# Kernel optimization log

Measured on AMD Instinct MI355X. Metric: run time of the kernel, lower is better.

## Reference

```python
import jax, jax.numpy as jnp
import numpy as np
from jax import lax

N_RAYS, N_STEPS, G = 4096, 160, 160
COLOR_DIM, WIDTH = 3, 128
POS_PE, VIEW_PE = 5, 4
XYZ_MIN, XYZ_MAX = -1.0, 1.0
NEAR = 0.05
STEPSIZE = 0.5
VOXEL_SIZE = (XYZ_MAX - XYZ_MIN) / G
DIST = STEPSIZE * VOXEL_SIZE
S_VAL = 80.0
FASTCOLOR_THRES = 1e-7
MASK_THRES = 1e-3
ALPHA_INIT = 1e-4
ACT_SHIFT = float(np.log(1.0 / (1.0 - ALPHA_INIT) - 1.0))
SMOOTH_K, SMOOTH_SIGMA = 5, 1.0
POSFREQ = jnp.asarray([2.0 ** i for i in range(POS_PE)], jnp.float32)
VIEWFREQ = jnp.asarray([2.0 ** i for i in range(VIEW_PE)], jnp.float32)


def _gauss_kernel():
    ax = np.arange(SMOOTH_K) - SMOOTH_K // 2
    g = np.exp(-(ax ** 2) / (2.0 * SMOOTH_SIGMA ** 2))
    k = g[:, None, None] * g[None, :, None] * g[None, None, :]
    return jnp.asarray(k / k.sum(), np.float32)[None, None]


def _trilerp(grid, pts):
    # grid [C,Gx,Gx,Gx]; pts [...,3] in world coords -> [..., C] (align_corners trilinear)
    Gx = grid.shape[-1]
    u = (pts - XYZ_MIN) / (XYZ_MAX - XYZ_MIN) * (Gx - 1)
    u = jnp.clip(u, 0.0, Gx - 1.0)
    i0 = jnp.clip(jnp.floor(u).astype(jnp.int32), 0, Gx - 2)
    f = u - i0.astype(u.dtype)
    x0, y0, z0 = i0[..., 0], i0[..., 1], i0[..., 2]
    fx, fy, fz = f[..., 0], f[..., 1], f[..., 2]
    def g8(ix, iy, iz):
        return grid[:, ix, iy, iz]  # [C, ...]
    out = (g8(x0, y0, z0) * (1 - fx) * (1 - fy) * (1 - fz)
         + g8(x0, y0, z0 + 1) * (1 - fx) * (1 - fy) * fz
         + g8(x0, y0 + 1, z0) * (1 - fx) * fy * (1 - fz)
         + g8(x0, y0 + 1, z0 + 1) * (1 - fx) * fy * fz
         + g8(x0 + 1, y0, z0) * fx * (1 - fy) * (1 - fz)
         + g8(x0 + 1, y0, z0 + 1) * fx * (1 - fy) * fz
         + g8(x0 + 1, y0 + 1, z0) * fx * fy * (1 - fz)
         + g8(x0 + 1, y0 + 1, z0 + 1) * fx * fy * fz)
    return jnp.moveaxis(out, 0, -1)


def _alphas2weights(alpha):
    # per-ray (segmented) exclusive cumprod of transmittance; alpha [N,S]
    T = jnp.cumprod(1.0 - alpha, axis=1)
    T_excl = jnp.concatenate([jnp.ones_like(T[:, :1]), T[:, :-1]], axis=1)
    return alpha * T_excl, T[:, -1]


def _mlp(x, w0, b0, w1, b1, w2, b2):
    h = jax.nn.relu(x @ w0 + b0)
    h = jax.nn.relu(h @ w1 + b1)
    return h @ w2 + b2


def _forward(rays_o, rays_d, viewdirs, sdf_grid, mask_density,
             off_color_grid, emo_color_grid,
             off_w0, off_b0, off_w1, off_b1, off_w2, off_b2,
             emo_w0, emo_b0, emo_w1, emo_b1, emo_w2, emo_b2, em_modes):
    N = rays_o.shape[0]
    t = NEAR + DIST * jnp.arange(N_STEPS, dtype=jnp.float32)
    ray_pts = rays_o[:, None, :] + rays_d[:, None, :] * t[None, :, None]  # [N,S,3]

    # MaskCache: threshold alpha from coarse density grid (boolean keep mask)
    dens = _trilerp(mask_density, ray_pts)[..., 0]
    mask_alpha = 1.0 - jnp.exp(-jax.nn.softplus(dens + ACT_SHIFT) * DIST)
    keep0 = mask_alpha >= MASK_THRES  # [N,S]

    # Gaussian-smoothed SDF grid + central-difference gradient grid
    sdf_s = lax.conv_general_dilated(sdf_grid, _gauss_kernel(), (1, 1, 1), 'SAME',
                                     dimension_numbers=('NCDHW', 'OIDHW', 'NCDHW'))[0]  # [1,G,G,G]
    s = sdf_s[0]
    grad_grid = jnp.zeros((3, G, G, G), sdf_grid.dtype)
    grad_grid = grad_grid.at[0, 1:-1].set((s[2:] - s[:-2]) / (2 * VOXEL_SIZE))
    grad_grid = grad_grid.at[1, :, 1:-1].set((s[:, 2:] - s[:, :-2]) / (2 * VOXEL_SIZE))
    grad_grid = grad_grid.at[2, :, :, 1:-1].set((s[:, :, 2:] - s[:, :, :-2]) / (2 * VOXEL_SIZE))

    sdf = _trilerp(sdf_s, ray_pts)[..., 0]   # [N,S]
    gradient = _trilerp(grad_grid, ray_pts)  # [N,S,3]

    # NeuS alpha from sdf (scatter, grad variant, cos_anneal = 1)
    true_cos = jnp.einsum('nd,nsd->ns', viewdirs, gradient)
    iter_cos = -jax.nn.relu(-true_cos)
    prev_cdf = jax.nn.sigmoid((sdf - iter_cos * DIST * 0.5) * S_VAL)
    next_cdf = jax.nn.sigmoid((sdf + iter_cos * DIST * 0.5) * S_VAL)
    alpha = jnp.clip((prev_cdf - next_cdf + 1e-5) / (prev_cdf + 1e-5), 0.0, 1.0)
    alpha = jnp.where(keep0, alpha, 0.0)  # masked points contribute nothing

    weights, _ = _alphas2weights(alpha)
    keep1 = weights > FASTCOLOR_THRES
    alpha = jnp.where(keep1, alpha, 0.0)
    weights, alphainv_last = _alphas2weights(alpha)

    # features: pos PE, view PE (per-ray, gathered by ray_id == broadcast), normal
    rays_xyz = (ray_pts - XYZ_MIN) / (XYZ_MAX - XYZ_MIN)  # [N,S,3]
    xyz_emb = (rays_xyz[..., None] * POSFREQ).reshape(N, N_STEPS, -1)
    v_emb = (viewdirs[..., None] * VIEWFREQ).reshape(N, -1)
    v_full = jnp.concatenate([v_emb, jnp.sin(v_emb), jnp.cos(v_emb)], -1)
    v_full = jnp.broadcast_to(v_full[:, None, :], (N, N_STEPS, v_full.shape[-1]))
    normal = gradient / (jnp.linalg.norm(gradient, axis=-1, keepdims=True) + 1e-5)
    rgb_feat = jnp.concatenate([rays_xyz, jnp.sin(xyz_emb), jnp.cos(xyz_emb), v_full, normal], -1)

    off_in = jnp.concatenate([_trilerp(off_color_grid, ray_pts), rgb_feat], -1)
    emo_in = jnp.concatenate([_trilerp(emo_color_grid, ray_pts), rgb_feat], -1)
    off_rgb = jax.nn.sigmoid(_mlp(off_in, off_w0, off_b0, off_w1, off_b1, off_w2, off_b2))
    emo_rgb = jax.nn.sigmoid(_mlp(emo_in, emo_w0, emo_b0, emo_w1, emo_b1, emo_w2, emo_b2))
    on_mask = (em_modes == 1)[:, None, None]  # em_modes[ray_id] == 1
    rgb = jnp.where(on_mask, emo_rgb, 0.0) + off_rgb

    w_ = weights[..., None]
    rgb_marched = jnp.sum(w_ * rgb, axis=1)  # segment_coo(sum over ray_id)
    cum_weights = jnp.sum(w_, axis=1)        # [N,1]
    return rgb_marched, alphainv_last, 1.0 - cum_weights


def setup_inputs() -> dict:
    key = jax.random.key(0)
    ks = jax.random.split(key, 12)
    rays_o = jax.random.uniform(ks[0], (N_RAYS, 3), jnp.float32, -0.3, 0.3)
    rd = jax.random.normal(ks[1], (N_RAYS, 3), jnp.float32)
    rays_d = rd / jnp.linalg.norm(rd, axis=-1, keepdims=True)
    viewdirs = rays_d
    em_modes = jax.random.randint(ks[2], (N_RAYS,), 0, 2)
    lin = np.linspace(-1.0, 1.0, G, dtype=np.float32)
    x, y, z = np.meshgrid(lin, lin, lin, indexing='ij')
    sdf_grid = jnp.asarray(np.sqrt(x ** 2 + y ** 2 + z ** 2) - 1.0)[None, None]  # sphere-SDF init
    mask_density = jax.random.normal(ks[3], (1, 80, 80, 80), jnp.float32) * 2.0 + 12.0
    off_color_grid = jax.random.normal(ks[4], (COLOR_DIM, G, G, G), jnp.float32) * 0.1
    emo_color_grid = jax.random.normal(ks[5], (COLOR_DIM, G, G, G), jnp.float32) * 0.1
    DIM0 = 3 + 3 * POS_PE * 2 + 3 * VIEW_PE * 3 + COLOR_DIM + 3  # = 75
    def lw(k, i, o):
        return jax.random.normal(k, (i, o), jnp.float32) * (1.0 / np.sqrt(i))
    return dict(rays_o=rays_o, rays_d=rays_d, viewdirs=viewdirs, em_modes=em_modes,
                sdf_grid=sdf_grid, mask_density=mask_density,
                off_color_grid=off_color_grid, emo_color_grid=emo_color_grid,
                off_w0=lw(ks[6], DIM0, WIDTH), off_b0=jnp.zeros((WIDTH,), jnp.float32),
                off_w1=lw(ks[7], WIDTH, WIDTH), off_b1=jnp.zeros((WIDTH,), jnp.float32),
                off_w2=lw(ks[8], WIDTH, 3), off_b2=jnp.zeros((3,), jnp.float32),
                emo_w0=lw(ks[9], DIM0, WIDTH), emo_b0=jnp.zeros((WIDTH,), jnp.float32),
                emo_w1=lw(ks[10], WIDTH, WIDTH), emo_b1=jnp.zeros((WIDTH,), jnp.float32),
                emo_w2=lw(ks[11], WIDTH, 3), emo_b2=jnp.zeros((3,), jnp.float32))


def reference(rays_o, rays_d, viewdirs, em_modes, sdf_grid, mask_density,
              off_color_grid, emo_color_grid,
              off_w0, off_b0, off_w1, off_b1, off_w2, off_b2,
              emo_w0, emo_b0, emo_w1, emo_b1, emo_w2, emo_b2):
    return _forward(rays_o, rays_d, viewdirs, sdf_grid, mask_density,
                    off_color_grid, emo_color_grid,
                    off_w0, off_b0, off_w1, off_b1, off_w2, off_b2,
                    emo_w0, emo_b0, emo_w1, emo_b1, emo_w2, emo_b2, em_modes)
```

## Files before the change

### kernel.cpp

```cpp
#include <hip/hip_runtime.h>

#define NRAYS 4096
#define NSTEPS 160
#define NSAMP (NRAYS*NSTEPS)
#define GG 160
#define GG2 (GG*GG)
#define GG3 (GG*GG2)
#define GM 80
#define GM2 (GM*GM)

#define NEARV 0.05f
#define DISTV 0.00625f
#define SVAL 80.0f
#define ACT_SHIFT_C (-9.2102403669758813f)
#define INV2H 40.0f
#define MASK_THRES_C 1e-3f
#define FAST_THRES_C 1e-7f

#define KW0 0.05448868454964295f
#define KW1 0.24420134200323332f
#define KW2 0.40261994689424750f

__device__ __forceinline__ float sigmf(float x){ return 1.0f/(1.0f+__expf(-x)); }
__device__ __forceinline__ float softplusf_(float x){ return (x>20.0f)? x : log1pf(__expf(x)); }

__device__ __forceinline__ void tricoord(float p, int Gx, int& i0, float& fr){
  float u = (p + 1.0f)*0.5f*(float)(Gx-1);
  u = fminf(fmaxf(u, 0.0f), (float)(Gx-1));
  int i = (int)floorf(u);
  i = min(max(i,0), Gx-2);
  i0 = i; fr = u - (float)i;
}

__global__ __launch_bounds__(256) void ksmooth_yz(const float* __restrict__ in, float* __restrict__ out,
                                                  float* __restrict__ outbuf, int* __restrict__ cnt){
  __shared__ float S[36][37];
  __shared__ float Tz[36][33];
  const int bx = blockIdx.x;
  const int t = threadIdx.x;
  if (bx == 0){
    for (int i = t; i < NRAYS*3; i += 256) outbuf[i] = 0.0f;
    if (t == 0) *cnt = 0;
  }
  const int x  = bx / 25;
  const int tile = bx % 25;
  const int Y0 = (tile/5)*32, Z0 = (tile%5)*32;
  const float kw[5] = {KW0,KW1,KW2,KW1,KW0};
  for (int i = t; i < 36*36; i += 256){
    int r = i/36, c = i - (i/36)*36;
    int y = Y0 + r - 2, z = Z0 + c - 2;
    float v = 0.0f;
    if (y>=0 && y<GG && z>=0 && z<GG) v = in[(x*GG+y)*GG+z];
    S[r][c] = v;
  }
  __syncthreads();
  for (int i = t; i < 36*32; i += 256){
    int r = i >> 5, c = i & 31;
    float acc = 0.f;
    #pragma unroll
    for (int d=0; d<5; d++) acc += kw[d]*S[r][c+d];
    Tz[r][c] = acc;
  }
  __syncthreads();
  for (int i = t; i < 32*32; i += 256){
    int yy = i >> 5, c = i & 31;
    float acc = 0.f;
    #pragma unroll
    for (int d=0; d<5; d++) acc += kw[d]*Tz[yy+d][c];
    out[(x*GG + Y0+yy)*GG + Z0 + c] = acc;
  }
}

__global__ __launch_bounds__(64) void kmarch(
  const float* __restrict__ ro, const float* __restrict__ rd,
  const float* __restrict__ vd, const float* __restrict__ maskg,
  const float* __restrict__ Y,
  int* __restrict__ slist, float* __restrict__ sw, float* __restrict__ sgrad,
  int* __restrict__ cnt, float* __restrict__ out)
{
  int n = blockIdx.x*64 + threadIdx.x;
  if (n >= NRAYS) return;
  const float ox=ro[n*3+0], oy=ro[n*3+1], oz=ro[n*3+2];
  const float dx=rd[n*3+0], dy=rd[n*3+1], dz=rd[n*3+2];
  const float vx=vd[n*3+0], vy=vd[n*3+1], vz=vd[n*3+2];
  const float kwc[5] = {KW0,KW1,KW2,KW1,KW0};
  float T1=1.0f, T2=1.0f, cum=0.0f;
  for (int s=0; s<NSTEPS; s++){
    float tt = NEARV + DISTV*(float)s;
    float px = ox + dx*tt, py = oy + dy*tt, pz = oz + dz*tt;

    int mx,my,mz; float mfx,mfy,mfz;
    tricoord(px, GM, mx, mfx); tricoord(py, GM, my, mfy); tricoord(pz, GM, mz, mfz);
    int mid = (mx*GM + my)*GM + mz;
    float d000=maskg[mid],        d001=maskg[mid+1];
    float d010=maskg[mid+GM],     d011=maskg[mid+GM+1];
    float d100=maskg[mid+GM2],    d101=maskg[mid+GM2+1];
    float d110=maskg[mid+GM2+GM], d111=maskg[mid+GM2+GM+1];
    float m00 = d000 + (d001-d000)*mfz;
    float m01 = d010 + (d011-d010)*mfz;
    float m10 = d100 + (d101-d100)*mfz;
    float m11 = d110 + (d111-d110)*mfz;
    float m0 = m00 + (m01-m00)*mfy;
    float m1 = m10 + (m11-m10)*mfy;
    float dens = m0 + (m1-m0)*mfx;
    float malpha = 1.0f - __expf(-softplusf_(dens + ACT_SHIFT_C)*DISTV);

    int ix,iy,iz; float fx,fy,fz;
    tricoord(px, GG, ix, fx); tricoord(py, GG, iy, fy); tricoord(pz, GG, iz, fz);

    float R[2][2][8];
    #pragma unroll
    for (int jb=0;jb<2;jb++)
      #pragma unroll
      for (int jc=0;jc<2;jc++)
        #pragma unroll
        for (int j=0;j<8;j++){
          int a = ix-3+j;
          R[jb][jc][j] = (a>=0 && a<GG) ? Y[(a*GG + iy+jb)*GG + iz+jc] : 0.0f;
        }
    const bool hasym = (iy>=1), hasyp = (iy<=GG-3);
    const bool haszm = (iz>=1), haszp = (iz<=GG-3);
    float Eym[2][6], Eyp[2][6], Ezm[2][6], Ezp[2][6];
    #pragma unroll
    for (int jc=0;jc<2;jc++)
      #pragma unroll
      for (int j=0;j<6;j++){
        int a = ix-2+j;
        bool ax = (a>=0 && a<GG);
        Eym[jc][j] = (hasym && ax) ? Y[(a*GG + iy-1)*GG + iz+jc] : 0.0f;
        Eyp[jc][j] = (hasyp && ax) ? Y[(a*GG + iy+2)*GG + iz+jc] : 0.0f;
      }
    #pragma unroll
    for (int jb=0;jb<2;jb++)
      #pragma unroll
      for (int j=0;j<6;j++){
        int a = ix-2+j;
        bool ax = (a>=0 && a<GG);
        Ezm[jb][j] = (haszm && ax) ? Y[(a*GG + iy+jb)*GG + iz-1] : 0.0f;
        Ezp[jb][j] = (haszp && ax) ? Y[(a*GG + iy+jb)*GG + iz+2] : 0.0f;
      }

    float sdf=0.0f, gx=0.0f, gy=0.0f, gz=0.0f;
    #pragma unroll
    for (int ja=0;ja<2;ja++){
      #pragma unroll
      for (int jb=0;jb<2;jb++){
        #pragma unroll
        for (int jc=0;jc<2;jc++){
          float w = (ja?fx:1.0f-fx)*(jb?fy:1.0f-fy)*(jc?fz:1.0f-fz);
          const float* r = R[jb][jc];
          float s0=0.0f;
          #pragma unroll
          for (int t2=0;t2<5;t2++) s0 += kwc[t2]*r[ja+1+t2];
          sdf += w*s0;
          int a = ix+ja, b = iy+jb, c = iz+jc;
          if (a>=1 && a<=GG-2){
            float sp=0.0f, sm=0.0f;
            #pragma unroll
            for (int t2=0;t2<5;t2++){ sp += kwc[t2]*r[ja+2+t2]; sm += kwc[t2]*r[ja+t2]; }
            gx += w*INV2H*(sp-sm);
          }
          if (b>=1 && b<=GG-2){
            float acc=0.0f;
            if (jb==0){
              const float* up = R[1][jc];
              const float* dn = Eym[jc];
              #pragma unroll
              for (int t2=0;t2<5;t2++) acc += kwc[t2]*(up[ja+1+t2] - dn[ja+t2]);
            } else {
              const float* up = Eyp[jc];
              const float* dn = R[0][jc];
              #pragma unroll
              for (int t2=0;t2<5;t2++) acc += kwc[t2]*(up[ja+t2] - dn[ja+1+t2]);
            }
            gy += w*INV2H*acc;
          }
          if (c>=1 && c<=GG-2){
            float acc=0.0f;
            if (jc==0){
              const float* up = R[jb][1];
              const float* dn = Ezm[jb];
              #pragma unroll
              for (int t2=0;t2<5;t2++) acc += kwc[t2]*(up[ja+1+t2] - dn[ja+t2]);
            } else {
              const float* up = Ezp[jb];
              const float* dn = R[jb][0];
              #pragma unroll
              for (int t2=0;t2<5;t2++) acc += kwc[t2]*(up[ja+t2] - dn[ja+1+t2]);
            }
            gz += w*INV2H*acc;
          }
        }
      }
    }

    float tc = vx*gx + vy*gy + vz*gz;
    float icos = fminf(tc, 0.0f);
    float e = icos*DISTV*0.5f;
    float prev = sigmf((sdf - e)*SVAL);
    float nxt  = sigmf((sdf + e)*SVAL);
    float alpha = (prev - nxt + 1e-5f)/(prev + 1e-5f);
    alpha = fminf(fmaxf(alpha, 0.0f), 1.0f);
    if (!(malpha >= MASK_THRES_C)) alpha = 0.0f;

    float w1 = alpha*T1; T1 *= (1.0f - alpha);
    float a2 = (w1 > FAST_THRES_C) ? alpha : 0.0f;
    float wv = a2*T2;   T2 *= (1.0f - a2);
    cum += wv;
    if (wv > 0.0f){
      int pos = atomicAdd(cnt, 1);
      slist[pos] = n*NSTEPS + s;
      sw[pos] = wv;
      sgrad[pos*3+0]=gx; sgrad[pos*3+1]=gy; sgrad[pos*3+2]=gz;
    }
    if (T1 <= FAST_THRES_C) break;
  }
  out[NRAYS*3 + n] = T2;
  out[NRAYS*4 + n] = 1.0f - cum;
}

__global__ __launch_bounds__(256) void kmlp5(
  const float* __restrict__ ro, const float* __restrict__ rd,
  const float* __restrict__ vd, const int* __restrict__ em,
  const float* __restrict__ offc, const float* __restrict__ emoc,
  const int* __restrict__ slist, const float* __restrict__ sw,
  const float* __restrict__ sgrad, const int* __restrict__ cnt,
  const float* __restrict__ W0o, const float* __restrict__ b0o,
  const float* __restrict__ W1o, const float* __restrict__ b1o,
  const float* __restrict__ W2o, const float* __restrict__ b2o,
  const float* __restrict__ W0e, const float* __restrict__ b0e,
  const float* __restrict__ W1e, const float* __restrict__ b1e,
  const float* __restrict__ W2e, const float* __restrict__ b2e,
  float* __restrict__ out)
{
  __shared__ float X[32][80];
  __shared__ float H[32][132];
  __shared__ float H2[32][132];
  __shared__ float OUTB[32][3];
  __shared__ float WSH[32];
  __shared__ float GS[32][3];
  __shared__ int SSAMP[32];
  __shared__ int SEM[32];
  __shared__ int s_go;

  const int t = threadIdx.x;
  const int count = *cnt;
  const int head = blockIdx.x & 1;
  const int cstride = gridDim.x >> 1;

  const float* W0 = head ? W0e : W0o;  const float* b0 = head ? b0e : b0o;
  const float* W1 = head ? W1e : W1o;  const float* b1 = head ? b1e : b1o;
  const float* W2 = head ? W2e : W2o;  const float* b2 = head ? b2e : b2o;
  const float* cg = head ? emoc : offc;
  const float4* W04 = (const float4*)W0;
  const float4* W14 = (const float4*)W1;

  const int lane = t & 31;
  const int sg   = t >> 5;

  for (int chunk = blockIdx.x >> 1; chunk*32 < count; chunk += cstride) {
    const int base = chunk*32;
    if (t == 0) s_go = 0;
    if (t < 32) {
      int i = base + t;
      bool vld = (i < count);
      int samp = vld ? slist[i] : 0;
      SSAMP[t] = samp;
      WSH[t]   = vld ? sw[i] : 0.0f;
      GS[t][0] = vld ? sgrad[i*3+0] : 0.0f;
      GS[t][1] = vld ? sgrad[i*3+1] : 0.0f;
      GS[t][2] = vld ? sgrad[i*3+2] : 0.0f;
      SEM[t]   = vld ? em[samp/NSTEPS] : 0;
    }
    __syncthreads();
    if (t < 32) {
      bool live = (WSH[t] > 0.0f) && (head == 0 || SEM[t] != 0);
      if (live) s_go = 1;
    }
    __syncthreads();

    if (s_go) {
      {
        const int s = t & 31;
        const int r = t >> 5;
        const int samp = SSAMP[s];
        const int n = samp / NSTEPS;
        const int step = samp - n*NSTEPS;
        const float tt = NEARV + DISTV*(float)step;
        const float px = ro[n*3+0] + rd[n*3+0]*tt;
        const float py = ro[n*3+1] + rd[n*3+1]*tt;
        const float pz = ro[n*3+2] + rd[n*3+2]*tt;
        if (r < 3) {
          int ix,iy,iz; float fx,fy,fz;
          tricoord(px, GG, ix, fx); tricoord(py, GG, iy, fy); tricoord(pz, GG, iz, fz);
          const float* g = cg + (size_t)r * GG3;
          const int id = (ix*GG + iy)*GG + iz;
          float v000=g[id],        v001=g[id+1];
          float v010=g[id+GG],     v011=g[id+GG+1];
          float v100=g[id+GG2],    v101=g[id+GG2+1];
          float v110=g[id+GG2+GG], v111=g[id+GG2+GG+1];
          float c00 = v000 + (v001-v000)*fz;
          float c01 = v010 + (v011-v010)*fz;
          float c10 = v100 + (v101-v100)*fz;
          float c11 = v110 + (v111-v110)*fz;
          float c0 = c00 + (c01-c00)*fy;
          float c1 = c10 + (c11-c10)*fy;
          X[s][r] = c0 + (c1-c0)*fx;
        } else if (r == 3) {
          X[s][3] = (px+1.0f)*0.5f;
          X[s][4] = (py+1.0f)*0.5f;
          X[s][5] = (pz+1.0f)*0.5f;
          float gx = GS[s][0], gy = GS[s][1], gz = GS[s][2];
          float inv = 1.0f/(sqrtf(gx*gx+gy*gy+gz*gz)+1e-5f);
          X[s][72] = gx*inv; X[s][73] = gy*inv; X[s][74] = gz*inv;
          X[s][75] = 0.0f; X[s][76] = 0.0f; X[s][77] = 0.0f; X[s][78] = 0.0f; X[s][79] = 0.0f;
        } else if (r < 7) {
          const int a = r - 4;
          const float coord = (a==0)?px:((a==1)?py:pz);
          const float rxyz = (coord+1.0f)*0.5f;
          float fr = 1.0f;
          #pragma unroll
          for (int q = 0; q < 5; q++) {
            float e = rxyz*fr; fr *= 2.0f;
            X[s][6  + a*5 + q] = __sinf(e);
            X[s][21 + a*5 + q] = __cosf(e);
          }
          const float v = vd[n*3+a];
          float fr2 = 1.0f;
          #pragma unroll
          for (int q = 0; q < 4; q++) {
            float e = v*fr2; fr2 *= 2.0f;
            X[s][36 + a*4 + q] = e;
            X[s][48 + a*4 + q] = __sinf(e);
            X[s][60 + a*4 + q] = __cosf(e);
          }
        }
      }
      __syncthreads();

      {
        const float4 bb = ((const float4*)b0)[lane];
        float4 a0 = bb, a1 = bb, a2 = bb, a3 = bb;
        const int s0 = sg*4;
        #pragma unroll 2
        for (int k4 = 0; k4 < 72; k4 += 4){
          float4 w0 = W04[(k4+0)*32 + lane];
          float4 w1 = W04[(k4+1)*32 + lane];
          float4 w2 = W04[(k4+2)*32 + lane];
          float4 w3 = W04[(k4+3)*32 + lane];
          float4 x0 = *(const float4*)&X[s0+0][k4];
          float4 x1 = *(const float4*)&X[s0+1][k4];
          float4 x2 = *(const float4*)&X[s0+2][k4];
          float4 x3 = *(const float4*)&X[s0+3][k4];
          a0.x+=x0.x*w0.x; a0.y+=x0.x*w0.y; a0.z+=x0.x*w0.z; a0.w+=x0.x*w0.w;
          a1.x+=x1.x*w0.x; a1.y+=x1.x*w0.y; a1.z+=x1.x*w0.z; a1.w+=x1.x*w0.w;
          a2.x+=x2.x*w0.x; a2.y+=x2.x*w0.y; a2.z+=x2.x*w0.z; a2.w+=x2.x*w0.w;
          a3.x+=x3.x*w0.x; a3.y+=x3.x*w0.y; a3.z+=x3.x*w0.z; a3.w+=x3.x*w0.w;
          a0.x+=x0.y*w1.x; a0.y+=x0.y*w1.y; a0.z+=x0.y*w1.z; a0.w+=x0.y*w1.w;
          a1.x+=x1.y*w1.x; a1.y+=x1.y*w1.y; a1.z+=x1.y*w1.z; a1.w+=x1.y*w1.w;
          a2.x+=x2.y*w1.x; a2.y+=x2.y*w1.y; a2.z+=x2.y*w1.z; a2.w+=x2.y*w1.w;
          a3.x+=x3.y*w1.x; a3.y+=x3.y*w1.y; a3.z+=x3.y*w1.z; a3.w+=x3.y*w1.w;
          a0.x+=x0.z*w2.x; a0.y+=x0.z*w2.y; a0.z+=x0.z*w2.z; a0.w+=x0.z*w2.w;
          a1.x+=x1.z*w2.x; a1.y+=x1.z*w2.y; a1.z+=x1.z*w2.z; a1.w+=x1.z*w2.w;
          a2.x+=x2.z*w2.x; a2.y+=x2.z*w2.y; a2.z+=x2.z*w2.z; a2.w+=x2.z*w2.w;
          a3.x+=x3.z*w2.x; a3.y+=x3.z*w2.y; a3.z+=x3.z*w2.z; a3.w+=x3.z*w2.w;
          a0.x+=x0.w*w3.x; a0.y+=x0.w*w3.y; a0.z+=x0.w*w3.z; a0.w+=x0.w*w3.w;
          a1.x+=x1.w*w3.x; a1.y+=x1.w*w3.y; a1.z+=x1.w*w3.z; a1.w+=x1.w*w3.w;
          a2.x+=x2.w*w3.x; a2.y+=x2.w*w3.y; a2.z+=x2.w*w3.z; a2.w+=x2.w*w3.w;
          a3.x+=x3.w*w3.x; a3.y+=x3.w*w3.y; a3.z+=x3.w*w3.z; a3.w+=x3.w*w3.w;
        }
        #pragma unroll
        for (int k = 72; k < 75; k++){
          float4 w = W04[k*32 + lane];
          float x0 = X[s0+0][k], x1 = X[s0+1][k], x2 = X[s0+2][k], x3 = X[s0+3][k];
          a0.x+=x0*w.x; a0.y+=x0*w.y; a0.z+=x0*w.z; a0.w+=x0*w.w;
          a1.x+=x1*w.x; a1.y+=x1*w.y; a1.z+=x1*w.z; a1.w+=x1*w.w;
          a2.x+=x2*w.x; a2.y+=x2*w.y; a2.z+=x2*w.z; a2.w+=x2*w.w;
          a3.x+=x3*w.x; a3.y+=x3*w.y; a3.z+=x3*w.z; a3.w+=x3*w.w;
        }
        H[s0+0][lane*4+0]=fmaxf(a0.x,0.f); H[s0+0][lane*4+1]=fmaxf(a0.y,0.f);
        H[s0+0][lane*4+2]=fmaxf(a0.z,0.f); H[s0+0][lane*4+3]=fmaxf(a0.w,0.f);
        H[s0+1][lane*4+0]=fmaxf(a1.x,0.f); H[s0+1][lane*4+1]=fmaxf(a1.y,0.f);
        H[s0+1][lane*4+2]=fmaxf(a1.z,0.f); H[s0+1][lane*4+3]=fmaxf(a1.w,0.f);
        H[s0+2][lane*4+0]=fmaxf(a2.x,0.f); H[s0+2][lane*4+1]=fmaxf(a2.y,0.f);
        H[s0+2][lane*4+2]=fmaxf(a2.z,0.f); H[s0+2][lane*4+3]=fmaxf(a2.w,0.f);
        H[s0+3][lane*4+0]=fmaxf(a3.x,0.f); H[s0+3][lane*4+1]=fmaxf(a3.y,0.f);
        H[s0+3][lane*4+2]=fmaxf(a3.z,0.f); H[s0+3][lane*4+3]=fmaxf(a3.w,0.f);
      }
      __syncthreads();

      {
        const float4 bb = ((const float4*)b1)[lane];
        float4 a0 = bb, a1 = bb, a2 = bb, a3 = bb;
        const int s0 = sg*4;
        #pragma unroll 2
        for (int k4 = 0; k4 < 128; k4 += 4){
          float4 w0 = W14[(k4+0)*32 + lane];
          float4 w1 = W14[(k4+1)*32 + lane];
          float4 w2 = W14[(k4+2)*32 + lane];
          float4 w3 = W14[(k4+3)*32 + lane];
          float4 x0 = *(const float4*)&H[s0+0][k4];
          float4 x1 = *(const float4*)&H[s0+1][k4];
          float4 x2 = *(const float4*)&H[s0+2][k4];
          float4 x3 = *(const float4*)&H[s0+3][k4];
          a0.x+=x0.x*w0.x; a0.y+=x0.x*w0.y; a0.z+=x0.x*w0.z; a0.w+=x0.x*w0.w;
          a1.x+=x1.x*w0.x; a1.y+=x1.x*w0.y; a1.z+=x1.x*w0.z; a1.w+=x1.x*w0.w;
          a2.x+=x2.x*w0.x; a2.y+=x2.x*w0.y; a2.z+=x2.x*w0.z; a2.w+=x2.x*w0.w;
          a3.x+=x3.x*w0.x; a3.y+=x3.x*w0.y; a3.z+=x3.x*w0.z; a3.w+=x3.x*w0.w;
          a0.x+=x0.y*w1.x; a0.y+=x0.y*w1.y; a0.z+=x0.y*w1.z; a0.w+=x0.y*w1.w;
          a1.x+=x1.y*w1.x; a1.y+=x1.y*w1.y; a1.z+=x1.y*w1.z; a1.w+=x1.y*w1.w;
          a2.x+=x2.y*w1.x; a2.y+=x2.y*w1.y; a2.z+=x2.y*w1.z; a2.w+=x2.y*w1.w;
          a3.x+=x3.y*w1.x; a3.y+=x3.y*w1.y; a3.z+=x3.y*w1.z; a3.w+=x3.y*w1.w;
          a0.x+=x0.z*w2.x; a0.y+=x0.z*w2.y; a0.z+=x0.z*w2.z; a0.w+=x0.z*w2.w;
          a1.x+=x1.z*w2.x; a1.y+=x1.z*w2.y; a1.z+=x1.z*w2.z; a1.w+=x1.z*w2.w;
          a2.x+=x2.z*w2.x; a2.y+=x2.z*w2.y; a2.z+=x2.z*w2.z; a2.w+=x2.z*w2.w;
          a3.x+=x3.z*w2.x; a3.y+=x3.z*w2.y; a3.z+=x3.z*w2.z; a3.w+=x3.z*w2.w;
          a0.x+=x0.w*w3.x; a0.y+=x0.w*w3.y; a0.z+=x0.w*w3.z; a0.w+=x0.w*w3.w;
          a1.x+=x1.w*w3.x; a1.y+=x1.w*w3.y; a1.z+=x1.w*w3.z; a1.w+=x1.w*w3.w;
          a2.x+=x2.w*w3.x; a2.y+=x2.w*w3.y; a2.z+=x2.w*w3.z; a2.w+=x2.w*w3.w;
          a3.x+=x3.w*w3.x; a3.y+=x3.w*w3.y; a3.z+=x3.w*w3.z; a3.w+=x3.w*w3.w;
        }
        H2[s0+0][lane*4+0]=fmaxf(a0.x,0.f); H2[s0+0][lane*4+1]=fmaxf(a0.y,0.f);
        H2[s0+0][lane*4+2]=fmaxf(a0.z,0.f); H2[s0+0][lane*4+3]=fmaxf(a0.w,0.f);
        H2[s0+1][lane*4+0]=fmaxf(a1.x,0.f); H2[s0+1][lane*4+1]=fmaxf(a1.y,0.f);
        H2[s0+1][lane*4+2]=fmaxf(a1.z,0.f); H2[s0+1][lane*4+3]=fmaxf(a1.w,0.f);
        H2[s0+2][lane*4+0]=fmaxf(a2.x,0.f); H2[s0+2][lane*4+1]=fmaxf(a2.y,0.f);
        H2[s0+2][lane*4+2]=fmaxf(a2.z,0.f); H2[s0+2][lane*4+3]=fmaxf(a2.w,0.f);
        H2[s0+3][lane*4+0]=fmaxf(a3.x,0.f); H2[s0+3][lane*4+1]=fmaxf(a3.y,0.f);
        H2[s0+3][lane*4+2]=fmaxf(a3.z,0.f); H2[s0+3][lane*4+3]=fmaxf(a3.w,0.f);
      }
      __syncthreads();

      {
        const int s0 = sg*4;
        #pragma unroll
        for (int i = 0; i < 4; i++){
          const int s = s0 + i;
          float4 h = *(const float4*)&H2[s][lane*4];
          float c0 = h.x*W2[(lane*4+0)*3+0] + h.y*W2[(lane*4+1)*3+0]
                   + h.z*W2[(lane*4+2)*3+0] + h.w*W2[(lane*4+3)*3+0];
          float c1 = h.x*W2[(lane*4+0)*3+1] + h.y*W2[(lane*4+1)*3+1]
                   + h.z*W2[(lane*4+2)*3+1] + h.w*W2[(lane*4+3)*3+1];
          float c2 = h.x*W2[(lane*4+0)*3+2] + h.y*W2[(lane*4+1)*3+2]
                   + h.z*W2[(lane*4+2)*3+2] + h.w*W2[(lane*4+3)*3+2];
          #pragma unroll
          for (int d=16; d>=1; d>>=1){
            c0 += __shfl_down(c0, d, 32);
            c1 += __shfl_down(c1, d, 32);
            c2 += __shfl_down(c2, d, 32);
          }
          if (lane == 0){
            OUTB[s][0] = sigmf(c0 + b2[0]);
            OUTB[s][1] = sigmf(c1 + b2[1]);
            OUTB[s][2] = sigmf(c2 + b2[2]);
          }
        }
      }
      __syncthreads();

      if (t < 96) {
        int s2 = t/3, c = t - s2*3;
        float w = WSH[s2];
        if (w > 0.0f && (head == 0 || SEM[s2] != 0)) {
          int n2 = SSAMP[s2]/NSTEPS;
          atomicAdd(&out[n2*3 + c], w * OUTB[s2][c]);
        }
      }
    }
    __syncthreads();
  }
}

extern "C" void kernel_launch(void* const* d_in, const int* in_sizes, int n_in,
                              void* d_out, int out_size, void* d_ws, size_t ws_size,
                              hipStream_t stream) {
  const float* ro    = (const float*)d_in[0];
  const float* rd    = (const float*)d_in[1];
  const float* vd    = (const float*)d_in[2];
  const int*   em    = (const int*)d_in[3];
  const float* sdfg  = (const float*)d_in[4];
  const float* maskg = (const float*)d_in[5];
  const float* offc  = (const float*)d_in[6];
  const float* emoc  = (const float*)d_in[7];
  const float* W0o = (const float*)d_in[8];
  const float* b0o = (const float*)d_in[9];
  const float* W1o = (const float*)d_in[10];
  const float* b1o = (const float*)d_in[11];
  const float* W2o = (const float*)d_in[12];
  const float* b2o = (const float*)d_in[13];
  const float* W0e = (const float*)d_in[14];
  const float* b0e = (const float*)d_in[15];
  const float* W1e = (const float*)d_in[16];
  const float* b1e = (const float*)d_in[17];
  const float* W2e = (const float*)d_in[18];
  const float* b2e = (const float*)d_in[19];

  float* out = (float*)d_out;
  float* ws  = (float*)d_ws;
  float* Yb    = ws;
  float* swb   = ws + GG3;
  float* sgradb= swb + NSAMP;
  int*   slist = (int*)(sgradb + 3*(size_t)NSAMP);
  int*   cnt   = slist + NSAMP;

  ksmooth_yz<<<GG*25, 256, 0, stream>>>(sdfg, Yb, out, cnt);

  kmarch<<<NRAYS/64, 64, 0, stream>>>(ro, rd, vd, maskg, Yb,
                                      slist, swb, sgradb, cnt, out);

  kmlp5<<<512, 256, 0, stream>>>(ro, rd, vd, em, offc, emoc,
                                 slist, swb, sgradb, cnt,
                                 W0o,b0o,W1o,b1o,W2o,b2o,
                                 W0e,b0e,W1e,b1e,W2e,b2e, out);
}
```

Before: 54.29 us.

## Partition surviving samples by emotion mode so emo-head skips inactive rays

The march kernel now writes samples from rays with em==1 from the back of the sample list, using a second counter, and the rest from the front. The emotion head iterates only over the em==1 segment, while the offset head covers both segments. This removes emo-MLP chunks that previously ran and were masked out. MLP chunks shrink from 32 to 16 samples and the grid doubles to 1024 blocks, with the view-encoding work moved onto spare thread rows. The risk is extra atomic contention on two counters and lower per-block reuse of the weight loads.

```diff
diff --git a/kernel.cpp b/kernel.cpp
--- a/kernel.cpp
+++ b/kernel.cpp
@@ -40,7 +40,7 @@
   const int t = threadIdx.x;
   if (bx == 0){
     for (int i = t; i < NRAYS*3; i += 256) outbuf[i] = 0.0f;
-    if (t == 0) *cnt = 0;
+    if (t < 2) cnt[t] = 0;
   }
   const int x  = bx / 25;
   const int tile = bx % 25;
@@ -73,8 +73,8 @@
 
 __global__ __launch_bounds__(64) void kmarch(
   const float* __restrict__ ro, const float* __restrict__ rd,
-  const float* __restrict__ vd, const float* __restrict__ maskg,
-  const float* __restrict__ Y,
+  const float* __restrict__ vd, const int* __restrict__ em,
+  const float* __restrict__ maskg, const float* __restrict__ Y,
   int* __restrict__ slist, float* __restrict__ sw, float* __restrict__ sgrad,
   int* __restrict__ cnt, float* __restrict__ out)
 {
@@ -83,6 +83,7 @@
   const float ox=ro[n*3+0], oy=ro[n*3+1], oz=ro[n*3+2];
   const float dx=rd[n*3+0], dy=rd[n*3+1], dz=rd[n*3+2];
   const float vx=vd[n*3+0], vy=vd[n*3+1], vz=vd[n*3+2];
+  const int emn = em[n];
   const float kwc[5] = {KW0,KW1,KW2,KW1,KW0};
   float T1=1.0f, T2=1.0f, cum=0.0f;
   for (int s=0; s<NSTEPS; s++){
@@ -208,7 +209,9 @@
     float wv = a2*T2;   T2 *= (1.0f - a2);
     cum += wv;
     if (wv > 0.0f){
-      int pos = atomicAdd(cnt, 1);
+      int pos;
+      if (emn == 1){ int p = atomicAdd(&cnt[1], 1); pos = NSAMP - 1 - p; }
+      else         { pos = atomicAdd(&cnt[0], 1); }
       slist[pos] = n*NSTEPS + s;
       sw[pos] = wv;
       sgrad[pos*3+0]=gx; sgrad[pos*3+1]=gy; sgrad[pos*3+2]=gz;
@@ -219,9 +222,9 @@
   out[NRAYS*4 + n] = 1.0f - cum;
 }
 
-__global__ __launch_bounds__(256) void kmlp5(
+__global__ __launch_bounds__(256) void kmlp6(
   const float* __restrict__ ro, const float* __restrict__ rd,
-  const float* __restrict__ vd, const int* __restrict__ em,
+  const float* __restrict__ vd,
   const float* __restrict__ offc, const float* __restrict__ emoc,
   const int* __restrict__ slist, const float* __restrict__ sw,
   const float* __restrict__ sgrad, const int* __restrict__ cnt,
@@ -233,20 +236,21 @@
   const float* __restrict__ W2e, const float* __restrict__ b2e,
   float* __restrict__ out)
 {
-  __shared__ float X[32][80];
-  __shared__ float H[32][132];
-  __shared__ float H2[32][132];
-  __shared__ float OUTB[32][3];
-  __shared__ float WSH[32];
-  __shared__ float GS[32][3];
-  __shared__ int SSAMP[32];
-  __shared__ int SEM[32];
-  __shared__ int s_go;
+  __shared__ float X[16][80];
+  __shared__ float H[16][132];
+  __shared__ float H2[16][132];
+  __shared__ float OUTB[16][3];
+  __shared__ float WSH[16];
+  __shared__ float GS[16][3];
+  __shared__ int SSAMP[16];
 
   const int t = threadIdx.x;
-  const int count = *cnt;
+  const int c0 = cnt[0];
+  const int c1 = cnt[1];
   const int head = blockIdx.x & 1;
   const int cstride = gridDim.x >> 1;
+  const int total = head ? c1 : (c0 + c1);
+  const int seg1 = NSAMP - c1;
 
   const float* W0 = head ? W0e : W0o;  const float* b0 = head ? b0e : b0o;
   const float* W1 = head ? W1e : W1o;  const float* b1 = head ? b1e : b1o;
@@ -258,213 +262,181 @@
   const int lane = t & 31;
   const int sg   = t >> 5;
 
-  for (int chunk = blockIdx.x >> 1; chunk*32 < count; chunk += cstride) {
-    const int base = chunk*32;
-    if (t == 0) s_go = 0;
-    if (t < 32) {
-      int i = base + t;
-      bool vld = (i < count);
+  for (int chunk = blockIdx.x >> 1; chunk*16 < total; chunk += cstride) {
+    const int base = chunk*16;
+    if (t < 16) {
+      int v = base + t;
+      bool vld = (v < total);
+      int i;
+      if (head) i = seg1 + v;
+      else      i = (v < c0) ? v : seg1 + (v - c0);
+      if (!vld) i = head ? seg1 : 0;
       int samp = vld ? slist[i] : 0;
       SSAMP[t] = samp;
       WSH[t]   = vld ? sw[i] : 0.0f;
       GS[t][0] = vld ? sgrad[i*3+0] : 0.0f;
       GS[t][1] = vld ? sgrad[i*3+1] : 0.0f;
       GS[t][2] = vld ? sgrad[i*3+2] : 0.0f;
-      SEM[t]   = vld ? em[samp/NSTEPS] : 0;
-    }
-    __syncthreads();
-    if (t < 32) {
-      bool live = (WSH[t] > 0.0f) && (head == 0 || SEM[t] != 0);
-      if (live) s_go = 1;
-    }
-    __syncthreads();
-
-    if (s_go) {
-      {
-        const int s = t & 31;
-        const int r = t >> 5;
-        const int samp = SSAMP[s];
-        const int n = samp / NSTEPS;
-        const int step = samp - n*NSTEPS;
-        const float tt = NEARV + DISTV*(float)step;
-        const float px = ro[n*3+0] + rd[n*3+0]*tt;
-        const float py = ro[n*3+1] + rd[n*3+1]*tt;
-        const float pz = ro[n*3+2] + rd[n*3+2]*tt;
-        if (r < 3) {
-          int ix,iy,iz; float fx,fy,fz;
-          tricoord(px, GG, ix, fx); tricoord(py, GG, iy, fy); tricoord(pz, GG, iz, fz);
-          const float* g = cg + (size_t)r * GG3;
-          const int id = (ix*GG + iy)*GG + iz;
-          float v000=g[id],        v001=g[id+1];
-          float v010=g[id+GG],     v011=g[id+GG+1];
-          float v100=g[id+GG2],    v101=g[id+GG2+1];
-          float v110=g[id+GG2+GG], v111=g[id+GG2+GG+1];
-          float c00 = v000 + (v001-v000)*fz;
-          float c01 = v010 + (v011-v010)*fz;
-          float c10 = v100 + (v101-v100)*fz;
-          float c11 = v110 + (v111-v110)*fz;
-          float c0 = c00 + (c01-c00)*fy;
-          float c1 = c10 + (c11-c10)*fy;
-          X[s][r] = c0 + (c1-c0)*fx;
-        } else if (r == 3) {
-          X[s][3] = (px+1.0f)*0.5f;
-          X[s][4] = (py+1.0f)*0.5f;
-          X[s][5] = (pz+1.0f)*0.5f;
-          float gx = GS[s][0], gy = GS[s][1], gz = GS[s][2];
-          float inv = 1.0f/(sqrtf(gx*gx+gy*gy+gz*gz)+1e-5f);
-          X[s][72] = gx*inv; X[s][73] = gy*inv; X[s][74] = gz*inv;
-          X[s][75] = 0.0f; X[s][76] = 0.0f; X[s][77] = 0.0f; X[s][78] = 0.0f; X[s][79] = 0.0f;
-        } else if (r < 7) {
-          const int a = r - 4;
-          const float coord = (a==0)?px:((a==1)?py:pz);
-          const float rxyz = (coord+1.0f)*0.5f;
-          float fr = 1.0f;
-          #pragma unroll
-          for (int q = 0; q < 5; q++) {
-            float e = rxyz*fr; fr *= 2.0f;
-            X[s][6  + a*5 + q] = __sinf(e);
-            X[s][21 + a*5 + q] = __cosf(e);
-          }
-          const float v = vd[n*3+a];
-          float fr2 = 1.0f;
-          #pragma unroll
-          for (int q = 0; q < 4; q++) {
-            float e = v*fr2; fr2 *= 2.0f;
-            X[s][36 + a*4 + q] = e;
-            X[s][48 + a*4 + q] = __sinf(e);
-            X[s][60 + a*4 + q] = __cosf(e);
-          }
-        }
-      }
-      __syncthreads();
-
-      {
-        const float4 bb = ((const float4*)b0)[lane];
-        float4 a0 = bb, a1 = bb, a2 = bb, a3 = bb;
-        const int s0 = sg*4;
-        #pragma unroll 2
-        for (int k4 = 0; k4 < 72; k4 += 4){
-          float4 w0 = W04[(k4+0)*32 + lane];
-          float4 w1 = W04[(k4+1)*32 + lane];
-          float4 w2 = W04[(k4+2)*32 + lane];
-          float4 w3 = W04[(k4+3)*32 + lane];
-          float4 x0 = *(const float4*)&X[s0+0][k4];
-          float4 x1 = *(const float4*)&X[s0+1][k4];
-          float4 x2 = *(const float4*)&X[s0+2][k4];
-          float4 x3 = *(const float4*)&X[s0+3][k4];
-          a0.x+=x0.x*w0.x; a0.y+=x0.x*w0.y; a0.z+=x0.x*w0.z; a0.w+=x0.x*w0.w;
-          a1.x+=x1.x*w0.x; a1.y+=x1.x*w0.y; a1.z+=x1.x*w0.z; a1.w+=x1.x*w0.w;
-          a2.x+=x2.x*w0.x; a2.y+=x2.x*w0.y; a2.z+=x2.x*w0.z; a2.w+=x2.x*w0.w;
-          a3.x+=x3.x*w0.x; a3.y+=x3.x*w0.y; a3.z+=x3.x*w0.z; a3.w+=x3.x*w0.w;
-          a0.x+=x0.y*w1.x; a0.y+=x0.y*w1.y; a0.z+=x0.y*w1.z; a0.w+=x0.y*w1.w;
-          a1.x+=x1.y*w1.x; a1.y+=x1.y*w1.y; a1.z+=x1.y*w1.z; a1.w+=x1.y*w1.w;
-          a2.x+=x2.y*w1.x; a2.y+=x2.y*w1.y; a2.z+=x2.y*w1.z; a2.w+=x2.y*w1.w;
-          a3.x+=x3.y*w1.x; a3.y+=x3.y*w1.y; a3.z+=x3.y*w1.z; a3.w+=x3.y*w1.w;
-          a0.x+=x0.z*w2.x; a0.y+=x0.z*w2.y; a0.z+=x0.z*w2.z; a0.w+=x0.z*w2.w;
-          a1.x+=x1.z*w2.x; a1.y+=x1.z*w2.y; a1.z+=x1.z*w2.z; a1.w+=x1.z*w2.w;
-          a2.x+=x2.z*w2.x; a2.y+=x2.z*w2.y; a2.z+=x2.z*w2.z; a2.w+=x2.z*w2.w;
-          a3.x+=x3.z*w2.x; a3.y+=x3.z*w2.y; a3.z+=x3.z*w2.z; a3.w+=x3.z*w2.w;
-          a0.x+=x0.w*w3.x; a0.y+=x0.w*w3.y; a0.z+=x0.w*w3.z; a0.w+=x0.w*w3.w;
-          a1.x+=x1.w*w3.x; a1.y+=x1.w*w3.y; a1.z+=x1.w*w3.z; a1.w+=x1.w*w3.w;
-          a2.x+=x2.w*w3.x; a2.y+=x2.w*w3.y; a2.z+=x2.w*w3.z; a2.w+=x2.w*w3.w;
-          a3.x+=x3.w*w3.x; a3.y+=x3.w*w3.y; a3.z+=x3.w*w3.z; a3.w+=x3.w*w3.w;
-        }
+    }
+    __syncthreads();
+
+    {
+      const int s = t & 15;
+      const int r = t >> 4;
+      const int samp = SSAMP[s];
+      const int n = samp / NSTEPS;
+      const int step = samp - n*NSTEPS;
+      const float tt = NEARV + DISTV*(float)step;
+      const float px = ro[n*3+0] + rd[n*3+0]*tt;
+      const float py = ro[n*3+1] + rd[n*3+1]*tt;
+      const float pz = ro[n*3+2] + rd[n*3+2]*tt;
+      if (r < 3) {
+        int ix,iy,iz; float fx,fy,fz;
+        tricoord(px, GG, ix, fx); tricoord(py, GG, iy, fy); tricoord(pz, GG, iz, fz);
+        const float* g = cg + (size_t)r * GG3;
+        const int id = (ix*GG + iy)*GG + iz;
+        float v000=g[id],        v001=g[id+1];
+        float v010=g[id+GG],     v011=g[id+GG+1];
+        float v100=g[id+GG2],    v101=g[id+GG2+1];
+        float v110=g[id+GG2+GG], v111=g[id+GG2+GG+1];
+        float c00 = v000 + (v001-v000)*fz;
+        float c01 = v010 + (v011-v010)*fz;
+        float c10 = v100 + (v101-v100)*fz;
+        float c11 = v110 + (v111-v110)*fz;
+        float cl0 = c00 + (c01-c00)*fy;
+        float cl1 = c10 + (c11-c10)*fy;
+        X[s][r] = cl0 + (cl1-cl0)*fx;
+      } else if (r == 3) {
+        X[s][3] = (px+1.0f)*0.5f;
+        X[s][4] = (py+1.0f)*0.5f;
+        X[s][5] = (pz+1.0f)*0.5f;
+        float gx = GS[s][0], gy = GS[s][1], gz = GS[s][2];
+        float inv = 1.0f/(sqrtf(gx*gx+gy*gy+gz*gz)+1e-5f);
+        X[s][72] = gx*inv; X[s][73] = gy*inv; X[s][74] = gz*inv;
+        X[s][75] = 0.0f; X[s][76] = 0.0f; X[s][77] = 0.0f; X[s][78] = 0.0f; X[s][79] = 0.0f;
+      } else if (r < 7) {
+        const int a = r - 4;
+        const float coord = (a==0)?px:((a==1)?py:pz);
+        const float rxyz = (coord+1.0f)*0.5f;
+        float fr = 1.0f;
         #pragma unroll
-        for (int k = 72; k < 75; k++){
-          float4 w = W04[k*32 + lane];
-          float x0 = X[s0+0][k], x1 = X[s0+1][k], x2 = X[s0+2][k], x3 = X[s0+3][k];
-          a0.x+=x0*w.x; a0.y+=x0*w.y; a0.z+=x0*w.z; a0.w+=x0*w.w;
-          a1.x+=x1*w.x; a1.y+=x1*w.y; a1.z+=x1*w.z; a1.w+=x1*w.w;
-          a2.x+=x2*w.x; a2.y+=x2*w.y; a2.z+=x2*w.z; a2.w+=x2*w.w;
-          a3.x+=x3*w.x; a3.y+=x3*w.y; a3.z+=x3*w.z; a3.w+=x3*w.w;
-        }
-        H[s0+0][lane*4+0]=fmaxf(a0.x,0.f); H[s0+0][lane*4+1]=fmaxf(a0.y,0.f);
-        H[s0+0][lane*4+2]=fmaxf(a0.z,0.f); H[s0+0][lane*4+3]=fmaxf(a0.w,0.f);
-        H[s0+1][lane*4+0]=fmaxf(a1.x,0.f); H[s0+1][lane*4+1]=fmaxf(a1.y,0.f);
-        H[s0+1][lane*4+2]=fmaxf(a1.z,0.f); H[s0+1][lane*4+3]=fmaxf(a1.w,0.f);
-        H[s0+2][lane*4+0]=fmaxf(a2.x,0.f); H[s0+2][lane*4+1]=fmaxf(a2.y,0.f);
-        H[s0+2][lane*4+2]=fmaxf(a2.z,0.f); H[s0+2][lane*4+3]=fmaxf(a2.w,0.f);
-        H[s0+3][lane*4+0]=fmaxf(a3.x,0.f); H[s0+3][lane*4+1]=fmaxf(a3.y,0.f);
-        H[s0+3][lane*4+2]=fmaxf(a3.z,0.f); H[s0+3][lane*4+3]=fmaxf(a3.w,0.f);
-      }
-      __syncthreads();
-
-      {
-        const float4 bb = ((const float4*)b1)[lane];
-        float4 a0 = bb, a1 = bb, a2 = bb, a3 = bb;
-        const int s0 = sg*4;
-        #pragma unroll 2
-        for (int k4 = 0; k4 < 128; k4 += 4){
-          float4 w0 = W14[(k4+0)*32 + lane];
-          float4 w1 = W14[(k4+1)*32 + lane];
-          float4 w2 = W14[(k4+2)*32 + lane];
-          float4 w3 = W14[(k4+3)*32 + lane];
-          float4 x0 = *(const float4*)&H[s0+0][k4];
-          float4 x1 = *(const float4*)&H[s0+1][k4];
-          float4 x2 = *(const float4*)&H[s0+2][k4];
-          float4 x3 = *(const float4*)&H[s0+3][k4];
-          a0.x+=x0.x*w0.x; a0.y+=x0.x*w0.y; a0.z+=x0.x*w0.z; a0.w+=x0.x*w0.w;
-          a1.x+=x1.x*w0.x; a1.y+=x1.x*w0.y; a1.z+=x1.x*w0.z; a1.w+=x1.x*w0.w;
-          a2.x+=x2.x*w0.x; a2.y+=x2.x*w0.y; a2.z+=x2.x*w0.z; a2.w+=x2.x*w0.w;
-          a3.x+=x3.x*w0.x; a3.y+=x3.x*w0.y; a3.z+=x3.x*w0.z; a3.w+=x3.x*w0.w;
-          a0.x+=x0.y*w1.x; a0.y+=x0.y*w1.y; a0.z+=x0.y*w1.z; a0.w+=x0.y*w1.w;
-          a1.x+=x1.y*w1.x; a1.y+=x1.y*w1.y; a1.z+=x1.y*w1.z; a1.w+=x1.y*w1.w;
-          a2.x+=x2.y*w1.x; a2.y+=x2.y*w1.y; a2.z+=x2.y*w1.z; a2.w+=x2.y*w1.w;
-          a3.x+=x3.y*w1.x; a3.y+=x3.y*w1.y; a3.z+=x3.y*w1.z; a3.w+=x3.y*w1.w;
-          a0.x+=x0.z*w2.x; a0.y+=x0.z*w2.y; a0.z+=x0.z*w2.z; a0.w+=x0.z*w2.w;
-          a1.x+=x1.z*w2.x; a1.y+=x1.z*w2.y; a1.z+=x1.z*w2.z; a1.w+=x1.z*w2.w;
-          a2.x+=x2.z*w2.x; a2.y+=x2.z*w2.y; a2.z+=x2.z*w2.z; a2.w+=x2.z*w2.w;
-          a3.x+=x3.z*w2.x; a3.y+=x3.z*w2.y; a3.z+=x3.z*w2.z; a3.w+=x3.z*w2.w;
-          a0.x+=x0.w*w3.x; a0.y+=x0.w*w3.y; a0.z+=x0.w*w3.z; a0.w+=x0.w*w3.w;
-          a1.x+=x1.w*w3.x; a1.y+=x1.w*w3.y; a1.z+=x1.w*w3.z; a1.w+=x1.w*w3.w;
-          a2.x+=x2.w*w3.x; a2.y+=x2.w*w3.y; a2.z+=x2.w*w3.z; a2.w+=x2.w*w3.w;
-          a3.x+=x3.w*w3.x; a3.y+=x3.w*w3.y; a3.z+=x3.w*w3.z; a3.w+=x3.w*w3.w;
-        }
-        H2[s0+0][lane*4+0]=fmaxf(a0.x,0.f); H2[s0+0][lane*4+1]=fmaxf(a0.y,0.f);
-        H2[s0+0][lane*4+2]=fmaxf(a0.z,0.f); H2[s0+0][lane*4+3]=fmaxf(a0.w,0.f);
-        H2[s0+1][lane*4+0]=fmaxf(a1.x,0.f); H2[s0+1][lane*4+1]=fmaxf(a1.y,0.f);
-        H2[s0+1][lane*4+2]=fmaxf(a1.z,0.f); H2[s0+1][lane*4+3]=fmaxf(a1.w,0.f);
-        H2[s0+2][lane*4+0]=fmaxf(a2.x,0.f); H2[s0+2][lane*4+1]=fmaxf(a2.y,0.f);
-        H2[s0+2][lane*4+2]=fmaxf(a2.z,0.f); H2[s0+2][lane*4+3]=fmaxf(a2.w,0.f);
-        H2[s0+3][lane*4+0]=fmaxf(a3.x,0.f); H2[s0+3][lane*4+1]=fmaxf(a3.y,0.f);
-        H2[s0+3][lane*4+2]=fmaxf(a3.z,0.f); H2[s0+3][lane*4+3]=fmaxf(a3.w,0.f);
-      }
-      __syncthreads();
-
-      {
-        const int s0 = sg*4;
+        for (int q = 0; q < 5; q++) {
+          float e = rxyz*fr; fr *= 2.0f;
+          X[s][6  + a*5 + q] = __sinf(e);
+          X[s][21 + a*5 + q] = __cosf(e);
+        }
+      } else if (r < 10) {
+        const int a = r - 7;
+        const int n2 = SSAMP[s] / NSTEPS;
+        const float v = vd[n2*3+a];
+        float fr = 1.0f;
         #pragma unroll
-        for (int i = 0; i < 4; i++){
-          const int s = s0 + i;
-          float4 h = *(const float4*)&H2[s][lane*4];
-          float c0 = h.x*W2[(lane*4+0)*3+0] + h.y*W2[(lane*4+1)*3+0]
-                   + h.z*W2[(lane*4+2)*3+0] + h.w*W2[(lane*4+3)*3+0];
-          float c1 = h.x*W2[(lane*4+0)*3+1] + h.y*W2[(lane*4+1)*3+1]
-                   + h.z*W2[(lane*4+2)*3+1] + h.w*W2[(lane*4+3)*3+1];
-          float c2 = h.x*W2[(lane*4+0)*3+2] + h.y*W2[(lane*4+1)*3+2]
-                   + h.z*W2[(lane*4+2)*3+2] + h.w*W2[(lane*4+3)*3+2];
-          #pragma unroll
-          for (int d=16; d>=1; d>>=1){
-            c0 += __shfl_down(c0, d, 32);
-            c1 += __shfl_down(c1, d, 32);
-            c2 += __shfl_down(c2, d, 32);
-          }
-          if (lane == 0){
-            OUTB[s][0] = sigmf(c0 + b2[0]);
-            OUTB[s][1] = sigmf(c1 + b2[1]);
-            OUTB[s][2] = sigmf(c2 + b2[2]);
-          }
-        }
-      }
-      __syncthreads();
-
-      if (t < 96) {
-        int s2 = t/3, c = t - s2*3;
-        float w = WSH[s2];
-        if (w > 0.0f && (head == 0 || SEM[s2] != 0)) {
-          int n2 = SSAMP[s2]/NSTEPS;
-          atomicAdd(&out[n2*3 + c], w * OUTB[s2][c]);
-        }
+        for (int q = 0; q < 4; q++) {
+          float e = v*fr; fr *= 2.0f;
+          X[s][36 + a*4 + q] = e;
+          X[s][48 + a*4 + q] = __sinf(e);
+          X[s][60 + a*4 + q] = __cosf(e);
+        }
+      }
+    }
+    __syncthreads();
+
+    {
+      const float4 bb = ((const float4*)b0)[lane];
+      float4 a0 = bb, a1 = bb;
+      const int s0 = sg*2;
+      #pragma unroll 3
+      for (int k4 = 0; k4 < 72; k4 += 4){
+        float4 w0 = W04[(k4+0)*32 + lane];
+        float4 w1 = W04[(k4+1)*32 + lane];
+        float4 w2 = W04[(k4+2)*32 + lane];
+        float4 w3 = W04[(k4+3)*32 + lane];
+        float4 x0 = *(const float4*)&X[s0+0][k4];
+        float4 x1 = *(const float4*)&X[s0+1][k4];
+        a0.x+=x0.x*w0.x; a0.y+=x0.x*w0.y; a0.z+=x0.x*w0.z; a0.w+=x0.x*w0.w;
+        a1.x+=x1.x*w0.x; a1.y+=x1.x*w0.y; a1.z+=x1.x*w0.z; a1.w+=x1.x*w0.w;
+        a0.x+=x0.y*w1.x; a0.y+=x0.y*w1.y; a0.z+=x0.y*w1.z; a0.w+=x0.y*w1.w;
+        a1.x+=x1.y*w1.x; a1.y+=x1.y*w1.y; a1.z+=x1.y*w1.z; a1.w+=x1.y*w1.w;
+        a0.x+=x0.z*w2.x; a0.y+=x0.z*w2.y; a0.z+=x0.z*w2.z; a0.w+=x0.z*w2.w;
+        a1.x+=x1.z*w2.x; a1.y+=x1.z*w2.y; a1.z+=x1.z*w2.z; a1.w+=x1.z*w2.w;
+        a0.x+=x0.w*w3.x; a0.y+=x0.w*w3.y; a0.z+=x0.w*w3.z; a0.w+=x0.w*w3.w;
+        a1.x+=x1.w*w3.x; a1.y+=x1.w*w3.y; a1.z+=x1.w*w3.z; a1.w+=x1.w*w3.w;
+      }
+      #pragma unroll
+      for (int k = 72; k < 75; k++){
+        float4 w = W04[k*32 + lane];
+        float x0 = X[s0+0][k], x1 = X[s0+1][k];
+        a0.x+=x0*w.x; a0.y+=x0*w.y; a0.z+=x0*w.z; a0.w+=x0*w.w;
+        a1.x+=x1*w.x; a1.y+=x1*w.y; a1.z+=x1*w.z; a1.w+=x1*w.w;
+      }
+      H[s0+0][lane*4+0]=fmaxf(a0.x,0.f); H[s0+0][lane*4+1]=fmaxf(a0.y,0.f);
+      H[s0+0][lane*4+2]=fmaxf(a0.z,0.f); H[s0+0][lane*4+3]=fmaxf(a0.w,0.f);
+      H[s0+1][lane*4+0]=fmaxf(a1.x,0.f); H[s0+1][lane*4+1]=fmaxf(a1.y,0.f);
+      H[s0+1][lane*4+2]=fmaxf(a1.z,0.f); H[s0+1][lane*4+3]=fmaxf(a1.w,0.f);
+    }
+    __syncthreads();
+
+    {
+      const float4 bb = ((const float4*)b1)[lane];
+      float4 a0 = bb, a1 = bb;
+      const int s0 = sg*2;
+      #pragma unroll 4
+      for (int k4 = 0; k4 < 128; k4 += 4){
+        float4 w0 = W14[(k4+0)*32 + lane];
+        float4 w1 = W14[(k4+1)*32 + lane];
+        float4 w2 = W14[(k4+2)*32 + lane];
+        float4 w3 = W14[(k4+3)*32 + lane];
+        float4 x0 = *(const float4*)&H[s0+0][k4];
+        float4 x1 = *(const float4*)&H[s0+1][k4];
+        a0.x+=x0.x*w0.x; a0.y+=x0.x*w0.y; a0.z+=x0.x*w0.z; a0.w+=x0.x*w0.w;
+        a1.x+=x1.x*w0.x; a1.y+=x1.x*w0.y; a1.z+=x1.x*w0.z; a1.w+=x1.x*w0.w;
+        a0.x+=x0.y*w1.x; a0.y+=x0.y*w1.y; a0.z+=x0.y*w1.z; a0.w+=x0.y*w1.w;
+        a1.x+=x1.y*w1.x; a1.y+=x1.y*w1.y; a1.z+=x1.y*w1.z; a1.w+=x1.y*w1.w;
+        a0.x+=x0.z*w2.x; a0.y+=x0.z*w2.y; a0.z+=x0.z*w2.z; a0.w+=x0.z*w2.w;
+        a1.x+=x1.z*w2.x; a1.y+=x1.z*w2.y; a1.z+=x1.z*w2.z; a1.w+=x1.z*w2.w;
+        a0.x+=x0.w*w3.x; a0.y+=x0.w*w3.y; a0.z+=x0.w*w3.z; a0.w+=x0.w*w3.w;
+        a1.x+=x1.w*w3.x; a1.y+=x1.w*w3.y; a1.z+=x1.w*w3.z; a1.w+=x1.w*w3.w;
+      }
+      H2[s0+0][lane*4+0]=fmaxf(a0.x,0.f); H2[s0+0][lane*4+1]=fmaxf(a0.y,0.f);
+      H2[s0+0][lane*4+2]=fmaxf(a0.z,0.f); H2[s0+0][lane*4+3]=fmaxf(a0.w,0.f);
+      H2[s0+1][lane*4+0]=fmaxf(a1.x,0.f); H2[s0+1][lane*4+1]=fmaxf(a1.y,0.f);
+      H2[s0+1][lane*4+2]=fmaxf(a1.z,0.f); H2[s0+1][lane*4+3]=fmaxf(a1.w,0.f);
+    }
+    __syncthreads();
+
+    {
+      const int s0 = sg*2;
+      #pragma unroll
+      for (int i = 0; i < 2; i++){
+        const int s = s0 + i;
+        float4 h = *(const float4*)&H2[s][lane*4];
+        float c0v = h.x*W2[(lane*4+0)*3+0] + h.y*W2[(lane*4+1)*3+0]
+                  + h.z*W2[(lane*4+2)*3+0] + h.w*W2[(lane*4+3)*3+0];
+        float c1v = h.x*W2[(lane*4+0)*3+1] + h.y*W2[(lane*4+1)*3+1]
+                  + h.z*W2[(lane*4+2)*3+1] + h.w*W2[(lane*4+3)*3+1];
+        float c2v = h.x*W2[(lane*4+0)*3+2] + h.y*W2[(lane*4+1)*3+2]
+                  + h.z*W2[(lane*4+2)*3+2] + h.w*W2[(lane*4+3)*3+2];
+        #pragma unroll
+        for (int d=16; d>=1; d>>=1){
+          c0v += __shfl_down(c0v, d, 32);
+          c1v += __shfl_down(c1v, d, 32);
+          c2v += __shfl_down(c2v, d, 32);
+        }
+        if (lane == 0){
+          OUTB[s][0] = sigmf(c0v + b2[0]);
+          OUTB[s][1] = sigmf(c1v + b2[1]);
+          OUTB[s][2] = sigmf(c2v + b2[2]);
+        }
+      }
+    }
+    __syncthreads();
+
+    if (t < 48) {
+      int s2 = t/3, c = t - s2*3;
+      float w = WSH[s2];
+      if (w > 0.0f) {
+        int n2 = SSAMP[s2]/NSTEPS;
+        atomicAdd(&out[n2*3 + c], w * OUTB[s2][c]);
       }
     }
     __syncthreads();
@@ -505,11 +477,11 @@
 
   ksmooth_yz<<<GG*25, 256, 0, stream>>>(sdfg, Yb, out, cnt);
 
-  kmarch<<<NRAYS/64, 64, 0, stream>>>(ro, rd, vd, maskg, Yb,
+  kmarch<<<NRAYS/64, 64, 0, stream>>>(ro, rd, vd, em, maskg, Yb,
                                       slist, swb, sgradb, cnt, out);
 
-  kmlp5<<<512, 256, 0, stream>>>(ro, rd, vd, em, offc, emoc,
-                                 slist, swb, sgradb, cnt,
-                                 W0o,b0o,W1o,b1o,W2o,b2o,
-                                 W0e,b0e,W1e,b1e,W2e,b2e, out);
+  kmlp6<<<1024, 256, 0, stream>>>(ro, rd, vd, offc, emoc,
+                                  slist, swb, sgradb, cnt,
+                                  W0o,b0o,W1o,b1o,W2o,b2o,
+                                  W0e,b0e,W1e,b1e,W2e,b2e, out);
 }
```

New measurement: 56.20 us. +3.5%, slower.
